# Performance work log

Hardware: AMD Instinct MI355X
Metric: run time of the kernel (lower is better)

## Reference

```python
import jax, jax.numpy as jnp
import numpy as np

N = 50000   # nodes
E = 300000  # edges
D = 256     # emb_dim
L = 5       # num_layers
BN_EPS = 1e-5


def setup_inputs() -> dict:
    key = jax.random.key(0)
    ks = jax.random.split(key, 6)
    scale = 0.05
    return {
        "x": jax.random.normal(ks[0], (N, D), jnp.float32),
        "src": jax.random.randint(ks[1], (E,), 0, N, dtype=jnp.int32),
        "dst": jax.random.randint(ks[2], (E,), 0, N, dtype=jnp.int32),
        "W1": jax.random.normal(ks[3], (L, D, D), jnp.float32) * scale,
        "b1": jnp.zeros((L, D), jnp.float32),
        "g1": jnp.ones((L, D), jnp.float32),
        "bt1": jnp.zeros((L, D), jnp.float32),
        "W2": jax.random.normal(ks[4], (L, D, D), jnp.float32) * scale,
        "b2": jnp.zeros((L, D), jnp.float32),
        "eps": jnp.zeros((L,), jnp.float32),
        "bn_g": jnp.ones((L, D), jnp.float32),
        "bn_b": jnp.zeros((L, D), jnp.float32),
    }


def _bn(h, gamma, beta):
    # torch BatchNorm1d training-mode forward: biased batch stats over nodes
    mean = jnp.mean(h, axis=0)
    var = jnp.var(h, axis=0)
    return (h - mean) * jax.lax.rsqrt(var + BN_EPS) * gamma + beta


def reference(x, src, dst, W1, b1, g1, bt1, W2, b2, eps, bn_g, bn_b):
    h = x
    for l in range(L):
        # GINConv: gather relu(x[src]) -> scatter-sum to dst
        msg = jax.nn.relu(h[src])                          # [E, D]
        agg = jax.ops.segment_sum(msg, dst, num_segments=N)  # [N, D]
        z = (1.0 + eps[l]) * h + agg
        # mlp: Linear -> BN -> ReLU -> Linear
        z = z @ W1[l] + b1[l]
        z = jax.nn.relu(_bn(z, g1[l], bt1[l]))
        z = z @ W2[l] + b2[l]
        # per-layer BatchNorm; dropout is identity (eval / drop_ratio=0)
        z = _bn(z, bn_g[l], bn_b[l])
        if l < L - 1:
            z = jax.nn.relu(z)
        h = z
    return h  # JK='last'
```

## Files before the change

kernel.cpp:

```cpp
#include <hip/hip_runtime.h>
#include <hip/hip_bf16.h>

#define N_NODES 50000
#define N_EDGES 300000
#define DIM 256
#define MPAD 50048

typedef __attribute__((ext_vector_type(8))) _Float16 half8;
typedef __attribute__((ext_vector_type(4))) _Float16 half4;
typedef __attribute__((ext_vector_type(4))) float f32x4;

__device__ __forceinline__ void async16(const void* g, void* l) {
    __builtin_amdgcn_global_load_lds(
        (const __attribute__((address_space(1))) unsigned int*)g,
        (__attribute__((address_space(3))) unsigned int*)l, 16, 0, 0);
}

__global__ __launch_bounds__(256) void hist_dst(const int* __restrict__ dst,
                                                int* __restrict__ deg, int E) {
    int e = blockIdx.x * blockDim.x + threadIdx.x;
    if (e < E) atomicAdd(&deg[dst[e]], 1);
}

__global__ __launch_bounds__(1024) void scan_blk(const int* __restrict__ deg,
                                                 int* __restrict__ ptr,
                                                 int* __restrict__ bsum, int n) {
    __shared__ int wsum[16];
    __shared__ int wpre[16];
    int tid = threadIdx.x;
    int i = blockIdx.x * 1024 + tid;
    int v = (i < n) ? deg[i] : 0;
    int lane = tid & 63, w = tid >> 6;
    int s = v;
#pragma unroll
    for (int off = 1; off < 64; off <<= 1) {
        int t = __shfl_up(s, off, 64);
        if (lane >= off) s += t;
    }
    if (lane == 63) wsum[w] = s;
    __syncthreads();
    if (tid < 16) {
        int acc = 0;
        for (int j = 0; j < tid; j++) acc += wsum[j];
        wpre[tid] = acc;
    }
    __syncthreads();
    int incl = s + wpre[w];
    if (i < n) ptr[i] = incl - v;
    if (tid == 1023) bsum[blockIdx.x] = incl;
}

__global__ __launch_bounds__(64) void scan_top(int* __restrict__ bsum,
                                               int* __restrict__ ptr,
                                               int nb, int n, int E) {
    int lane = threadIdx.x;
    int v = (lane < nb) ? bsum[lane] : 0;
    int s = v;
#pragma unroll
    for (int off = 1; off < 64; off <<= 1) {
        int t = __shfl_up(s, off, 64);
        if (lane >= off) s += t;
    }
    if (lane < nb) bsum[lane] = s - v;
    if (lane == 0) ptr[n] = E;
}

__global__ __launch_bounds__(1024) void scan_add(int* __restrict__ ptr,
                                                 const int* __restrict__ bsum,
                                                 int* __restrict__ cursor, int n) {
    int i = blockIdx.x * 1024 + threadIdx.x;
    if (i < n) {
        int val = ptr[i] + bsum[blockIdx.x];
        ptr[i] = val;
        cursor[i] = val;
    }
}

__global__ __launch_bounds__(256) void scatter_src(const int* __restrict__ src,
                                                   const int* __restrict__ dst,
                                                   int* __restrict__ cursor,
                                                   int* __restrict__ srcbuf, int E) {
    int e = blockIdx.x * blockDim.x + threadIdx.x;
    if (e < E) {
        int pos = atomicAdd(&cursor[dst[e]], 1);
        srcbuf[pos] = src[e];
    }
}

__global__ __launch_bounds__(256) void x2h(const float* __restrict__ x,
                                           _Float16* __restrict__ hb) {
    size_t i = (size_t)blockIdx.x * 256 + threadIdx.x;
    float4 v = ((const float4*)x)[i];
    half4 o;
    o.x = (_Float16)v.x; o.y = (_Float16)v.y;
    o.z = (_Float16)v.z; o.w = (_Float16)v.w;
    ((half4*)hb)[i] = o;
}

__global__ __launch_bounds__(256) void wconv(const float* __restrict__ W1,
                                             const float* __restrict__ W2,
                                             _Float16* __restrict__ Wt) {
    int mat = blockIdx.x >> 4;
    int t = blockIdx.x & 15;
    int tr = t >> 2, tc = t & 3;
    const float* W = (mat < 5) ? (W1 + (size_t)mat * 65536)
                               : (W2 + (size_t)(mat - 5) * 65536);
    __shared__ float tile[64][65];
    int tid = threadIdx.x;
    int c = tid & 63, r0 = tid >> 6;
#pragma unroll 4
    for (int i = 0; i < 16; i++) {
        int r = r0 + i * 4;
        tile[r][c] = W[(size_t)(tr * 64 + r) * 256 + tc * 64 + c];
    }
    __syncthreads();
    _Float16* o = Wt + (size_t)mat * 65536;
#pragma unroll 4
    for (int i = 0; i < 16; i++) {
        int r = r0 + i * 4;
        o[(size_t)(tc * 64 + r) * 256 + tr * 64 + c] = (_Float16)tile[c][r];
    }
}

__global__ __launch_bounds__(256) void gather_h(const _Float16* __restrict__ h,
                                                const int* __restrict__ ptr,
                                                const int* __restrict__ srcbuf,
                                                _Float16* __restrict__ z,
                                                const float* __restrict__ eps) {
    int node = blockIdx.x * 4 + (threadIdx.x >> 6);
    if (node >= N_NODES) return;
    int lane = threadIdx.x & 63;
    int beg = ptr[node], end = ptr[node + 1];
    float s = 1.0f + eps[0];
    half4 hv = ((const half4*)(h + (size_t)node * DIM))[lane];
    float a0 = (float)hv.x * s, a1 = (float)hv.y * s;
    float a2 = (float)hv.z * s, a3 = (float)hv.w * s;
    int e = beg;
    for (; e + 4 <= end; e += 4) {
        int s0 = srcbuf[e], s1 = srcbuf[e + 1], s2 = srcbuf[e + 2], s3 = srcbuf[e + 3];
        half4 v0 = ((const half4*)(h + (size_t)s0 * DIM))[lane];
        half4 v1 = ((const half4*)(h + (size_t)s1 * DIM))[lane];
        half4 v2 = ((const half4*)(h + (size_t)s2 * DIM))[lane];
        half4 v3 = ((const half4*)(h + (size_t)s3 * DIM))[lane];
        a0 += fmaxf((float)v0.x, 0.f) + fmaxf((float)v1.x, 0.f)
            + fmaxf((float)v2.x, 0.f) + fmaxf((float)v3.x, 0.f);
        a1 += fmaxf((float)v0.y, 0.f) + fmaxf((float)v1.y, 0.f)
            + fmaxf((float)v2.y, 0.f) + fmaxf((float)v3.y, 0.f);
        a2 += fmaxf((float)v0.z, 0.f) + fmaxf((float)v1.z, 0.f)
            + fmaxf((float)v2.z, 0.f) + fmaxf((float)v3.z, 0.f);
        a3 += fmaxf((float)v0.w, 0.f) + fmaxf((float)v1.w, 0.f)
            + fmaxf((float)v2.w, 0.f) + fmaxf((float)v3.w, 0.f);
    }
    for (; e < end; e++) {
        half4 v = ((const half4*)(h + (size_t)srcbuf[e] * DIM))[lane];
        a0 += fmaxf((float)v.x, 0.f); a1 += fmaxf((float)v.y, 0.f);
        a2 += fmaxf((float)v.z, 0.f); a3 += fmaxf((float)v.w, 0.f);
    }
    half4 o;
    o.x = (_Float16)a0; o.y = (_Float16)a1;
    o.z = (_Float16)a2; o.w = (_Float16)a3;
    ((half4*)(z + (size_t)node * DIM))[lane] = o;
}

__global__ __launch_bounds__(256) void gather_bn(const _Float16* __restrict__ C,
                                                 const int* __restrict__ ptr,
                                                 const int* __restrict__ srcbuf,
                                                 _Float16* __restrict__ z,
                                                 const float* __restrict__ scsh,
                                                 const float* __restrict__ eps,
                                                 int l) {
    int node = blockIdx.x * 4 + (threadIdx.x >> 6);
    if (node >= N_NODES) return;
    int lane = threadIdx.x & 63;
    float4 sc = ((const float4*)scsh)[lane];
    float4 sh = ((const float4*)(scsh + DIM))[lane];
    int beg = ptr[node], end = ptr[node + 1];
    float s = 1.0f + eps[l];
    half4 hv = ((const half4*)(C + (size_t)node * DIM))[lane];
    float a0 = s * fmaxf((float)hv.x * sc.x + sh.x, 0.f);
    float a1 = s * fmaxf((float)hv.y * sc.y + sh.y, 0.f);
    float a2 = s * fmaxf((float)hv.z * sc.z + sh.z, 0.f);
    float a3 = s * fmaxf((float)hv.w * sc.w + sh.w, 0.f);
    int e = beg;
    for (; e + 4 <= end; e += 4) {
        int s0 = srcbuf[e], s1 = srcbuf[e + 1], s2 = srcbuf[e + 2], s3 = srcbuf[e + 3];
        half4 v0 = ((const half4*)(C + (size_t)s0 * DIM))[lane];
        half4 v1 = ((const half4*)(C + (size_t)s1 * DIM))[lane];
        half4 v2 = ((const half4*)(C + (size_t)s2 * DIM))[lane];
        half4 v3 = ((const half4*)(C + (size_t)s3 * DIM))[lane];
        a0 += fmaxf((float)v0.x * sc.x + sh.x, 0.f) + fmaxf((float)v1.x * sc.x + sh.x, 0.f)
            + fmaxf((float)v2.x * sc.x + sh.x, 0.f) + fmaxf((float)v3.x * sc.x + sh.x, 0.f);
        a1 += fmaxf((float)v0.y * sc.y + sh.y, 0.f) + fmaxf((float)v1.y * sc.y + sh.y, 0.f)
            + fmaxf((float)v2.y * sc.y + sh.y, 0.f) + fmaxf((float)v3.y * sc.y + sh.y, 0.f);
        a2 += fmaxf((float)v0.z * sc.z + sh.z, 0.f) + fmaxf((float)v1.z * sc.z + sh.z, 0.f)
            + fmaxf((float)v2.z * sc.z + sh.z, 0.f) + fmaxf((float)v3.z * sc.z + sh.z, 0.f);
        a3 += fmaxf((float)v0.w * sc.w + sh.w, 0.f) + fmaxf((float)v1.w * sc.w + sh.w, 0.f)
            + fmaxf((float)v2.w * sc.w + sh.w, 0.f) + fmaxf((float)v3.w * sc.w + sh.w, 0.f);
    }
    for (; e < end; e++) {
        half4 v = ((const half4*)(C + (size_t)srcbuf[e] * DIM))[lane];
        a0 += fmaxf((float)v.x * sc.x + sh.x, 0.f);
        a1 += fmaxf((float)v.y * sc.y + sh.y, 0.f);
        a2 += fmaxf((float)v.z * sc.z + sh.z, 0.f);
        a3 += fmaxf((float)v.w * sc.w + sh.w, 0.f);
    }
    half4 o;
    o.x = (_Float16)a0; o.y = (_Float16)a1;
    o.z = (_Float16)a2; o.w = (_Float16)a3;
    ((half4*)(z + (size_t)node * DIM))[lane] = o;
}

__global__ __launch_bounds__(256) void gemm_f16(const _Float16* __restrict__ A,
                                                const _Float16* __restrict__ Wt,
                                                const float* __restrict__ bias,
                                                _Float16* __restrict__ C,
                                                float* __restrict__ stats,
                                                int M) {
    __shared__ _Float16 Asm[128 * 32];
    __shared__ _Float16 Bsm[128 * 32];
    __shared__ float colsum[128];
    __shared__ float colsq[128];

    int tid = threadIdx.x;
    int wid = tid >> 6, lane = tid & 63;
    int quad = lane >> 4, lrow = lane & 15;
    int row0 = blockIdx.y * 128, col0 = blockIdx.x * 128;
    int wm = (wid & 1) * 64, wn = (wid >> 1) * 64;

    if (tid < 128) { colsum[tid] = 0.0f; colsq[tid] = 0.0f; }

    f32x4 acc[4][4] = {};
    const char* Ab = (const char*)A;
    const char* Bb = (const char*)Wt;

    for (int k0 = 0; k0 < DIM; k0 += 32) {
#pragma unroll
        for (int j = 0; j < 2; j++) {
            int b = wid * 2048 + j * 1024 + lane * 16;
            int m = b >> 6;
            int kb = b & 63;
            async16(Ab + (size_t)(row0 + m) * 512 + k0 * 2 + kb,
                    (char*)Asm + wid * 2048 + j * 1024);
            async16(Bb + (size_t)(col0 + m) * 512 + k0 * 2 + kb,
                    (char*)Bsm + wid * 2048 + j * 1024);
        }
        __syncthreads();

        half8 af[4], bf[4];
#pragma unroll
        for (int t = 0; t < 4; t++) {
            af[t] = *(const half8*)(Asm + (wm + t * 16 + lrow) * 32 + quad * 8);
            bf[t] = *(const half8*)(Bsm + (wn + t * 16 + lrow) * 32 + quad * 8);
        }
#pragma unroll
        for (int i = 0; i < 4; i++)
#pragma unroll
            for (int j = 0; j < 4; j++)
                acc[i][j] = __builtin_amdgcn_mfma_f32_16x16x32_f16(
                    af[i], bf[j], acc[i][j], 0, 0, 0);
        __syncthreads();
    }

    float bcol[4];
#pragma unroll
    for (int j = 0; j < 4; j++) bcol[j] = bias[col0 + wn + j * 16 + lrow];

    float csum[4] = {0.f, 0.f, 0.f, 0.f};
    float csq[4] = {0.f, 0.f, 0.f, 0.f};
#pragma unroll
    for (int i = 0; i < 4; i++) {
        int rbase = row0 + wm + i * 16 + quad * 4;
#pragma unroll
        for (int j = 0; j < 4; j++) {
            int col = col0 + wn + j * 16 + lrow;
#pragma unroll
            for (int r = 0; r < 4; r++) {
                int row = rbase + r;
                if (row < M) {
                    float v = acc[i][j][r] + bcol[j];
                    C[(size_t)row * DIM + col] = (_Float16)v;
                    csum[j] += v;
                    csq[j] += v * v;
                }
            }
        }
    }
#pragma unroll
    for (int j = 0; j < 4; j++) {
        atomicAdd(&colsum[wn + j * 16 + lrow], csum[j]);
        atomicAdd(&colsq[wn + j * 16 + lrow], csq[j]);
    }
    __syncthreads();
    if (tid < 128) {
        atomicAdd(&stats[col0 + tid], colsum[tid]);
        atomicAdd(&stats[DIM + col0 + tid], colsq[tid]);
    }
}

__global__ __launch_bounds__(256) void gemm_bn(const _Float16* __restrict__ A,
                                               const _Float16* __restrict__ Wt,
                                               const float* __restrict__ bias,
                                               const float* __restrict__ scsh,
                                               _Float16* __restrict__ C,
                                               float* __restrict__ stats,
                                               int M) {
    __shared__ _Float16 Asm[128 * 32];
    __shared__ _Float16 Bsm[128 * 32];
    __shared__ _Float16 scs[DIM];
    __shared__ _Float16 shs[DIM];
    __shared__ float colsum[128];
    __shared__ float colsq[128];

    int tid = threadIdx.x;
    int wid = tid >> 6, lane = tid & 63;
    int quad = lane >> 4, lrow = lane & 15;
    int row0 = blockIdx.y * 128, col0 = blockIdx.x * 128;
    int wm = (wid & 1) * 64, wn = (wid >> 1) * 64;

    scs[tid] = (_Float16)scsh[tid];
    shs[tid] = (_Float16)scsh[DIM + tid];
    if (tid < 128) { colsum[tid] = 0.0f; colsq[tid] = 0.0f; }

    f32x4 acc[4][4] = {};
    const char* Ab = (const char*)A;
    const char* Bb = (const char*)Wt;
    const half8 zerov = {0, 0, 0, 0, 0, 0, 0, 0};

    for (int k0 = 0; k0 < DIM; k0 += 32) {
#pragma unroll
        for (int j = 0; j < 2; j++) {
            int b = wid * 2048 + j * 1024 + lane * 16;
            int m = b >> 6;
            int kb = b & 63;
            async16(Ab + (size_t)(row0 + m) * 512 + k0 * 2 + kb,
                    (char*)Asm + wid * 2048 + j * 1024);
            async16(Bb + (size_t)(col0 + m) * 512 + k0 * 2 + kb,
                    (char*)Bsm + wid * 2048 + j * 1024);
        }
        __syncthreads();

        half8 scv = *(const half8*)(scs + k0 + quad * 8);
        half8 shv = *(const half8*)(shs + k0 + quad * 8);

        half8 af[4], bf[4];
#pragma unroll
        for (int t = 0; t < 4; t++) {
            half8 a = *(const half8*)(Asm + (wm + t * 16 + lrow) * 32 + quad * 8);
            af[t] = __builtin_elementwise_max(a * scv + shv, zerov);
            bf[t] = *(const half8*)(Bsm + (wn + t * 16 + lrow) * 32 + quad * 8);
        }
#pragma unroll
        for (int i = 0; i < 4; i++)
#pragma unroll
            for (int j = 0; j < 4; j++)
                acc[i][j] = __builtin_amdgcn_mfma_f32_16x16x32_f16(
                    af[i], bf[j], acc[i][j], 0, 0, 0);
        __syncthreads();
    }

    float bcol[4];
#pragma unroll
    for (int j = 0; j < 4; j++) bcol[j] = bias[col0 + wn + j * 16 + lrow];

    float csum[4] = {0.f, 0.f, 0.f, 0.f};
    float csq[4] = {0.f, 0.f, 0.f, 0.f};
#pragma unroll
    for (int i = 0; i < 4; i++) {
        int rbase = row0 + wm + i * 16 + quad * 4;
#pragma unroll
        for (int j = 0; j < 4; j++) {
            int col = col0 + wn + j * 16 + lrow;
#pragma unroll
            for (int r = 0; r < 4; r++) {
                int row = rbase + r;
                if (row < M) {
                    float v = acc[i][j][r] + bcol[j];
                    C[(size_t)row * DIM + col] = (_Float16)v;
                    csum[j] += v;
                    csq[j] += v * v;
                }
            }
        }
    }
#pragma unroll
    for (int j = 0; j < 4; j++) {
        atomicAdd(&colsum[wn + j * 16 + lrow], csum[j]);
        atomicAdd(&colsq[wn + j * 16 + lrow], csq[j]);
    }
    __syncthreads();
    if (tid < 128) {
        atomicAdd(&stats[col0 + tid], colsum[tid]);
        atomicAdd(&stats[DIM + col0 + tid], colsq[tid]);
    }
}

__global__ __launch_bounds__(256) void bn_finalize(float* __restrict__ stats,
                                                   const float* __restrict__ g,
                                                   const float* __restrict__ beta,
                                                   float* __restrict__ scsh,
                                                   int n) {
    int d = threadIdx.x;
    float invn = 1.0f / (float)n;
    float mean = stats[d] * invn;
    float var = stats[DIM + d] * invn - mean * mean;
    float inv = rsqrtf(var + 1e-5f);
    float scale = g[d] * inv;
    scsh[d] = scale;
    scsh[DIM + d] = beta[d] - mean * scale;
    stats[d] = 0.0f;
    stats[DIM + d] = 0.0f;
}

__global__ __launch_bounds__(256) void bn_apply_f(const _Float16* __restrict__ in,
                                                  float* __restrict__ outf,
                                                  const float* __restrict__ scsh) {
    size_t i = (size_t)blockIdx.x * 256 + threadIdx.x;
    int c4 = (int)(i & 63);
    float4 sc = ((const float4*)scsh)[c4];
    float4 sh = ((const float4*)(scsh + DIM))[c4];
    half4 v = ((const half4*)in)[i];
    float4 o;
    o.x = (float)v.x * sc.x + sh.x;
    o.y = (float)v.y * sc.y + sh.y;
    o.z = (float)v.z * sc.z + sh.z;
    o.w = (float)v.w * sc.w + sh.w;
    ((float4*)outf)[i] = o;
}

extern "C" void kernel_launch(void* const* d_in, const int* in_sizes, int n_in,
                              void* d_out, int out_size, void* d_ws, size_t ws_size,
                              hipStream_t stream) {
    (void)in_sizes; (void)n_in; (void)out_size; (void)ws_size;
    const float* x   = (const float*)d_in[0];
    const int*   src = (const int*)d_in[1];
    const int*   dst = (const int*)d_in[2];
    const float* W1  = (const float*)d_in[3];
    const float* b1  = (const float*)d_in[4];
    const float* g1  = (const float*)d_in[5];
    const float* bt1 = (const float*)d_in[6];
    const float* W2  = (const float*)d_in[7];
    const float* b2  = (const float*)d_in[8];
    const float* eps = (const float*)d_in[9];
    const float* bng = (const float*)d_in[10];
    const float* bnb = (const float*)d_in[11];
    float* out = (float*)d_out;

    const int N = N_NODES, E = N_EDGES, D = DIM;
    size_t NDp = (size_t)MPAD * D;

    _Float16* gin  = (_Float16*)d_ws;
    _Float16* C1   = gin + NDp;
    _Float16* C2   = C1 + NDp;
    _Float16* Wt   = C2 + NDp;
    float* stats = (float*)(Wt + 10 * 65536);
    float* scshA = stats + 1024;
    float* scshB = scshA + 512;
    int* deg     = (int*)(scshB + 512);
    int* ptr     = deg + N;
    int* bsum    = ptr + N + 1;
    int* srcbuf  = bsum + 64;

    const int ELEM4_BLOCKS = N * D / 4 / 256;
    const int NODE_BLOCKS  = (N + 3) / 4;
    const int E_BLOCKS     = (E + 255) / 256;
    const int SCAN_BLOCKS  = (N + 1023) / 1024;
    const dim3 GEMM_GRID(2, MPAD / 128);

    hipMemsetAsync(deg, 0, N * sizeof(int), stream);
    hipMemsetAsync(stats, 0, 1024 * sizeof(float), stream);
    hist_dst<<<E_BLOCKS, 256, 0, stream>>>(dst, deg, E);
    scan_blk<<<SCAN_BLOCKS, 1024, 0, stream>>>(deg, ptr, bsum, N);
    scan_top<<<1, 64, 0, stream>>>(bsum, ptr, SCAN_BLOCKS, N, E);
    scan_add<<<SCAN_BLOCKS, 1024, 0, stream>>>(ptr, bsum, deg, N);
    scatter_src<<<E_BLOCKS, 256, 0, stream>>>(src, dst, deg, srcbuf, E);
    wconv<<<160, 256, 0, stream>>>(W1, W2, Wt);
    x2h<<<ELEM4_BLOCKS, 256, 0, stream>>>(x, C1);

    for (int l = 0; l < 5; l++) {
        if (l == 0)
            gather_h<<<NODE_BLOCKS, 256, 0, stream>>>(C1, ptr, srcbuf, gin, eps);
        else
            gather_bn<<<NODE_BLOCKS, 256, 0, stream>>>(C2, ptr, srcbuf, gin,
                                                       scshB, eps, l);

        gemm_f16<<<GEMM_GRID, 256, 0, stream>>>(
            gin, Wt + (size_t)l * 65536, b1 + (size_t)l * D, C1, stats, N);
        bn_finalize<<<1, 256, 0, stream>>>(stats, g1 + (size_t)l * D,
                                           bt1 + (size_t)l * D, scshA, N);

        gemm_bn<<<GEMM_GRID, 256, 0, stream>>>(
            C1, Wt + (size_t)(5 + l) * 65536, b2 + (size_t)l * D, scshA,
            C2, stats + 512, N);
        bn_finalize<<<1, 256, 0, stream>>>(stats + 512, bng + (size_t)l * D,
                                           bnb + (size_t)l * D, scshB, N);

        if (l == 4)
            bn_apply_f<<<ELEM4_BLOCKS, 256, 0, stream>>>(C2, out, scshB);
    }
}
```

Measured before the change: 746.2 us.

## Use 128-wide K tiles with XOR-swizzled LDS in both GEMM kernels

Both GEMM kernels now stage K in two 128-wide chunks in a single 64KB shared buffer instead of eight 32-wide chunks. This cuts the number of barriers and load rounds per tile. LDS placement uses an XOR swizzle on 16-byte chunks to avoid bank conflicts on the wider rows. The BN scale/shift values are held in registers rather than shared memory, and the column-stat scratch reuses the GEMM buffer in a shared epilogue macro. The cost is much more LDS per block, which likely lowers occupancy, plus extra registers for the scale/shift vectors.

Result: faster. 727.7 us (-2.5%).

```diff
diff --git a/kernel.cpp b/kernel.cpp
--- a/kernel.cpp
+++ b/kernel.cpp
@@ -210,16 +210,53 @@
     ((half4*)(z + (size_t)node * DIM))[lane] = o;
 }
 
+#define GEMM_EPILOGUE(DOSTATS)                                               \
+    __syncthreads();                                                         \
+    float* colsum = (float*)smem;                                            \
+    float* colsq = colsum + 128;                                             \
+    if (tid < 128) { colsum[tid] = 0.0f; colsq[tid] = 0.0f; }                \
+    __syncthreads();                                                         \
+    float bcol[4];                                                           \
+    _Pragma("unroll")                                                        \
+    for (int j = 0; j < 4; j++) bcol[j] = bias[col0 + wn + j * 16 + lrow];   \
+    float csum[4] = {0.f, 0.f, 0.f, 0.f};                                    \
+    float csq[4] = {0.f, 0.f, 0.f, 0.f};                                     \
+    _Pragma("unroll")                                                        \
+    for (int i = 0; i < 4; i++) {                                            \
+        int rbase = row0 + wm + i * 16 + quad * 4;                           \
+        _Pragma("unroll")                                                    \
+        for (int j = 0; j < 4; j++) {                                        \
+            int col = col0 + wn + j * 16 + lrow;                             \
+            _Pragma("unroll")                                                \
+            for (int r = 0; r < 4; r++) {                                    \
+                int row = rbase + r;                                         \
+                if (row < M) {                                               \
+                    float v = acc[i][j][r] + bcol[j];                        \
+                    C[(size_t)row * DIM + col] = (_Float16)v;                \
+                    csum[j] += v;                                            \
+                    csq[j] += v * v;                                         \
+                }                                                            \
+            }                                                                \
+        }                                                                    \
+    }                                                                        \
+    _Pragma("unroll")                                                        \
+    for (int j = 0; j < 4; j++) {                                            \
+        atomicAdd(&colsum[wn + j * 16 + lrow], csum[j]);                     \
+        atomicAdd(&colsq[wn + j * 16 + lrow], csq[j]);                       \
+    }                                                                        \
+    __syncthreads();                                                         \
+    if (tid < 128) {                                                         \
+        atomicAdd(&stats[col0 + tid], colsum[tid]);                          \
+        atomicAdd(&stats[DIM + col0 + tid], colsq[tid]);                     \
+    }
+
 __global__ __launch_bounds__(256) void gemm_f16(const _Float16* __restrict__ A,
                                                 const _Float16* __restrict__ Wt,
                                                 const float* __restrict__ bias,
                                                 _Float16* __restrict__ C,
                                                 float* __restrict__ stats,
                                                 int M) {
-    __shared__ _Float16 Asm[128 * 32];
-    __shared__ _Float16 Bsm[128 * 32];
-    __shared__ float colsum[128];
-    __shared__ float colsq[128];
+    __shared__ uint4 smem[4096];
 
     int tid = threadIdx.x;
     int wid = tid >> 6, lane = tid & 63;
@@ -227,74 +264,49 @@
     int row0 = blockIdx.y * 128, col0 = blockIdx.x * 128;
     int wm = (wid & 1) * 64, wn = (wid >> 1) * 64;
 
-    if (tid < 128) { colsum[tid] = 0.0f; colsq[tid] = 0.0f; }
-
     f32x4 acc[4][4] = {};
     const char* Ab = (const char*)A;
     const char* Bb = (const char*)Wt;
 
-    for (int k0 = 0; k0 < DIM; k0 += 32) {
-#pragma unroll
-        for (int j = 0; j < 2; j++) {
-            int b = wid * 2048 + j * 1024 + lane * 16;
-            int m = b >> 6;
-            int kb = b & 63;
-            async16(Ab + (size_t)(row0 + m) * 512 + k0 * 2 + kb,
-                    (char*)Asm + wid * 2048 + j * 1024);
-            async16(Bb + (size_t)(col0 + m) * 512 + k0 * 2 + kb,
-                    (char*)Bsm + wid * 2048 + j * 1024);
+#pragma unroll
+    for (int ko = 0; ko < 2; ko++) {
+        int kb0 = ko * 256;
+#pragma unroll
+        for (int j = 0; j < 8; j++) {
+            int sbase = wid * 512 + j * 64;
+            int s = sbase + lane;
+            int m = s >> 4;
+            int c = (s & 15) ^ (m & 7);
+            size_t go = (size_t)(row0 + m) * 512 + kb0 + c * 16;
+            async16(Ab + go, (char*)smem + sbase * 16);
+            size_t gob = (size_t)(col0 + m) * 512 + kb0 + c * 16;
+            async16(Bb + gob, (char*)smem + 32768 + sbase * 16);
         }
         __syncthreads();
-
-        half8 af[4], bf[4];
-#pragma unroll
-        for (int t = 0; t < 4; t++) {
-            af[t] = *(const half8*)(Asm + (wm + t * 16 + lrow) * 32 + quad * 8);
-            bf[t] = *(const half8*)(Bsm + (wn + t * 16 + lrow) * 32 + quad * 8);
+#pragma unroll
+        for (int kc = 0; kc < 4; kc++) {
+            half8 af[4], bf[4];
+#pragma unroll
+            for (int t = 0; t < 4; t++) {
+                int ma = wm + t * 16 + lrow;
+                int ca = kc * 4 + quad;
+                af[t] = *(const half8*)((const char*)smem +
+                                        (ma * 16 + (ca ^ (ma & 7))) * 16);
+                int mb = wn + t * 16 + lrow;
+                bf[t] = *(const half8*)((const char*)smem + 32768 +
+                                        (mb * 16 + (ca ^ (mb & 7))) * 16);
+            }
+#pragma unroll
+            for (int i = 0; i < 4; i++)
+#pragma unroll
+                for (int j2 = 0; j2 < 4; j2++)
+                    acc[i][j2] = __builtin_amdgcn_mfma_f32_16x16x32_f16(
+                        af[i], bf[j2], acc[i][j2], 0, 0, 0);
         }
-#pragma unroll
-        for (int i = 0; i < 4; i++)
-#pragma unroll
-            for (int j = 0; j < 4; j++)
-                acc[i][j] = __builtin_amdgcn_mfma_f32_16x16x32_f16(
-                    af[i], bf[j], acc[i][j], 0, 0, 0);
-        __syncthreads();
-    }
-
-    float bcol[4];
-#pragma unroll
-    for (int j = 0; j < 4; j++) bcol[j] = bias[col0 + wn + j * 16 + lrow];
-
-    float csum[4] = {0.f, 0.f, 0.f, 0.f};
-    float csq[4] = {0.f, 0.f, 0.f, 0.f};
-#pragma unroll
-    for (int i = 0; i < 4; i++) {
-        int rbase = row0 + wm + i * 16 + quad * 4;
-#pragma unroll
-        for (int j = 0; j < 4; j++) {
-            int col = col0 + wn + j * 16 + lrow;
-#pragma unroll
-            for (int r = 0; r < 4; r++) {
-                int row = rbase + r;
-                if (row < M) {
-                    float v = acc[i][j][r] + bcol[j];
-                    C[(size_t)row * DIM + col] = (_Float16)v;
-                    csum[j] += v;
-                    csq[j] += v * v;
-                }
-            }
-        }
-    }
-#pragma unroll
-    for (int j = 0; j < 4; j++) {
-        atomicAdd(&colsum[wn + j * 16 + lrow], csum[j]);
-        atomicAdd(&colsq[wn + j * 16 + lrow], csq[j]);
-    }
-    __syncthreads();
-    if (tid < 128) {
-        atomicAdd(&stats[col0 + tid], colsum[tid]);
-        atomicAdd(&stats[DIM + col0 + tid], colsq[tid]);
-    }
+        if (ko == 0) __syncthreads();
+    }
+
+    GEMM_EPILOGUE(1)
 }
 
 __global__ __launch_bounds__(256) void gemm_bn(const _Float16* __restrict__ A,
@@ -304,12 +316,7 @@
                                                _Float16* __restrict__ C,
                                                float* __restrict__ stats,
                                                int M) {
-    __shared__ _Float16 Asm[128 * 32];
-    __shared__ _Float16 Bsm[128 * 32];
-    __shared__ _Float16 scs[DIM];
-    __shared__ _Float16 shs[DIM];
-    __shared__ float colsum[128];
-    __shared__ float colsq[128];
+    __shared__ uint4 smem[4096];
 
     int tid = threadIdx.x;
     int wid = tid >> 6, lane = tid & 63;
@@ -317,81 +324,69 @@
     int row0 = blockIdx.y * 128, col0 = blockIdx.x * 128;
     int wm = (wid & 1) * 64, wn = (wid >> 1) * 64;
 
-    scs[tid] = (_Float16)scsh[tid];
-    shs[tid] = (_Float16)scsh[DIM + tid];
-    if (tid < 128) { colsum[tid] = 0.0f; colsq[tid] = 0.0f; }
+    half8 scv[8], shv[8];
+#pragma unroll
+    for (int cc = 0; cc < 8; cc++) {
+        int kk = cc * 32 + quad * 8;
+        float4 s0 = *(const float4*)(scsh + kk);
+        float4 s1 = *(const float4*)(scsh + kk + 4);
+        float4 h0 = *(const float4*)(scsh + DIM + kk);
+        float4 h1 = *(const float4*)(scsh + DIM + kk + 4);
+        half8 sv = {(_Float16)s0.x, (_Float16)s0.y, (_Float16)s0.z, (_Float16)s0.w,
+                    (_Float16)s1.x, (_Float16)s1.y, (_Float16)s1.z, (_Float16)s1.w};
+        half8 hv = {(_Float16)h0.x, (_Float16)h0.y, (_Float16)h0.z, (_Float16)h0.w,
+                    (_Float16)h1.x, (_Float16)h1.y, (_Float16)h1.z, (_Float16)h1.w};
+        scv[cc] = sv;
+        shv[cc] = hv;
+    }
 
     f32x4 acc[4][4] = {};
     const char* Ab = (const char*)A;
     const char* Bb = (const char*)Wt;
     const half8 zerov = {0, 0, 0, 0, 0, 0, 0, 0};
 
-    for (int k0 = 0; k0 < DIM; k0 += 32) {
-#pragma unroll
-        for (int j = 0; j < 2; j++) {
-            int b = wid * 2048 + j * 1024 + lane * 16;
-            int m = b >> 6;
-            int kb = b & 63;
-            async16(Ab + (size_t)(row0 + m) * 512 + k0 * 2 + kb,
-                    (char*)Asm + wid * 2048 + j * 1024);
-            async16(Bb + (size_t)(col0 + m) * 512 + k0 * 2 + kb,
-                    (char*)Bsm + wid * 2048 + j * 1024);
+#pragma unroll
+    for (int ko = 0; ko < 2; ko++) {
+        int kb0 = ko * 256;
+#pragma unroll
+        for (int j = 0; j < 8; j++) {
+            int sbase = wid * 512 + j * 64;
+            int s = sbase + lane;
+            int m = s >> 4;
+            int c = (s & 15) ^ (m & 7);
+            size_t go = (size_t)(row0 + m) * 512 + kb0 + c * 16;
+            async16(Ab + go, (char*)smem + sbase * 16);
+            size_t gob = (size_t)(col0 + m) * 512 + kb0 + c * 16;
+            async16(Bb + gob, (char*)smem + 32768 + sbase * 16);
         }
         __syncthreads();
-
-        half8 scv = *(const half8*)(scs + k0 + quad * 8);
-        half8 shv = *(const half8*)(shs + k0 + quad * 8);
-
-        half8 af[4], bf[4];
-#pragma unroll
-        for (int t = 0; t < 4; t++) {
-            half8 a = *(const half8*)(Asm + (wm + t * 16 + lrow) * 32 + quad * 8);
-            af[t] = __builtin_elementwise_max(a * scv + shv, zerov);
-            bf[t] = *(const half8*)(Bsm + (wn + t * 16 + lrow) * 32 + quad * 8);
+#pragma unroll
+        for (int kc = 0; kc < 4; kc++) {
+            half8 af[4], bf[4];
+            half8 sv = scv[ko * 4 + kc];
+            half8 hv = shv[ko * 4 + kc];
+#pragma unroll
+            for (int t = 0; t < 4; t++) {
+                int ma = wm + t * 16 + lrow;
+                int ca = kc * 4 + quad;
+                half8 a = *(const half8*)((const char*)smem +
+                                          (ma * 16 + (ca ^ (ma & 7))) * 16);
+                af[t] = __builtin_elementwise_max(a * sv + hv, zerov);
+                int mb = wn + t * 16 + lrow;
+                bf[t] = *(const half8*)((const char*)smem + 32768 +
+                                        (mb * 16 + (ca ^ (mb & 7))) * 16);
+            }
+#pragma unroll
+            for (int i = 0; i < 4; i++)
+#pragma unroll
+                for (int j2 = 0; j2 < 4; j2++)
+                    acc[i][j2] = __builtin_amdgcn_mfma_f32_16x16x32_f16(
+                        af[i], bf[j2], acc[i][j2], 0, 0, 0);
         }
-#pragma unroll
-        for (int i = 0; i < 4; i++)
-#pragma unroll
-            for (int j = 0; j < 4; j++)
-                acc[i][j] = __builtin_amdgcn_mfma_f32_16x16x32_f16(
-                    af[i], bf[j], acc[i][j], 0, 0, 0);
-        __syncthreads();
-    }
-
-    float bcol[4];
-#pragma unroll
-    for (int j = 0; j < 4; j++) bcol[j] = bias[col0 + wn + j * 16 + lrow];
-
-    float csum[4] = {0.f, 0.f, 0.f, 0.f};
-    float csq[4] = {0.f, 0.f, 0.f, 0.f};
-#pragma unroll
-    for (int i = 0; i < 4; i++) {
-        int rbase = row0 + wm + i * 16 + quad * 4;
-#pragma unroll
-        for (int j = 0; j < 4; j++) {
-            int col = col0 + wn + j * 16 + lrow;
-#pragma unroll
-            for (int r = 0; r < 4; r++) {
-                int row = rbase + r;
-                if (row < M) {
-                    float v = acc[i][j][r] + bcol[j];
-                    C[(size_t)row * DIM + col] = (_Float16)v;
-                    csum[j] += v;
-                    csq[j] += v * v;
-                }
-            }
-        }
-    }
-#pragma unroll
-    for (int j = 0; j < 4; j++) {
-        atomicAdd(&colsum[wn + j * 16 + lrow], csum[j]);
-        atomicAdd(&colsq[wn + j * 16 + lrow], csq[j]);
-    }
-    __syncthreads();
-    if (tid < 128) {
-        atomicAdd(&stats[col0 + tid], colsum[tid]);
-        atomicAdd(&stats[DIM + col0 + tid], colsq[tid]);
-    }
+        if (ko == 0) __syncthreads();
+    }
+
+    GEMM_EPILOGUE(1)
 }
 
 __global__ __launch_bounds__(256) void bn_finalize(float* __restrict__ stats,
```
